# Optimization experiments

Hardware: AMD Instinct MI355X
Metric: run time of the kernel (lower is better)

The kernel has to match this reference:

```python
import jax, jax.numpy as jnp
import numpy as np

N_NODES = 100000
N_EDGES = 1600000
D_IN = 64
D_HID = 64
D_OUT = 64
DROP_P = 0.5


def _degree_norms(src, dst, n):
    ones = jnp.ones(src.shape[0], dtype=jnp.float32)
    deg_out = jax.ops.segment_sum(ones, src, num_segments=n)  # out-degree of src nodes
    deg_in = jax.ops.segment_sum(ones, dst, num_segments=n)   # in-degree of dst nodes
    norm_src = jnp.where(deg_out > 0, jax.lax.rsqrt(jnp.maximum(deg_out, 1.0)), 0.0)
    norm_dst = jnp.where(deg_in > 0, jax.lax.rsqrt(jnp.maximum(deg_in, 1.0)), 0.0)
    return norm_src, norm_dst


def _graph_conv(h, W, b, src, dst, norm_src, norm_dst, n, activation=None):
    # DGL GraphConv, norm='both': out = D_in^{-1/2} A (D_out^{-1/2} h) W + b
    h = h * norm_src[:, None]
    h = h @ W                      # small GEMM first (in >= out), math-equivalent
    msg = h[src]                   # gather  [E, d]
    agg = jax.ops.segment_sum(msg, dst, num_segments=n)  # scatter-add [N, d]
    out = agg * norm_dst[:, None] + b
    if activation is not None:
        out = activation(out)
    return out


def _dropout(h, key, p=DROP_P):
    keep = jax.random.bernoulli(key, 1.0 - p, h.shape)
    return jnp.where(keep, h / (1.0 - p), 0.0)


def setup_inputs() -> dict:
    key = jax.random.key(0)
    ks = jax.random.split(key, 6)
    x = jax.random.normal(ks[0], (N_NODES, D_IN), dtype=jnp.float32)
    W0 = jax.random.normal(ks[1], (D_IN, D_HID), dtype=jnp.float32) * 0.05
    W1 = jax.random.normal(ks[2], (D_HID, D_HID), dtype=jnp.float32) * 0.05
    W2 = jax.random.normal(ks[3], (D_HID, D_OUT), dtype=jnp.float32) * 0.05
    b0 = jnp.zeros((D_HID,), dtype=jnp.float32)
    b1 = jnp.zeros((D_HID,), dtype=jnp.float32)
    b2 = jnp.zeros((D_OUT,), dtype=jnp.float32)
    src = jax.random.randint(ks[4], (N_EDGES,), 0, N_NODES, dtype=jnp.int32)
    dst = jax.random.randint(ks[5], (N_EDGES,), 0, N_NODES, dtype=jnp.int32)
    return {"x": x, "W0": W0, "b0": b0, "W1": W1, "b1": b1, "W2": W2, "b2": b2,
            "src": src, "dst": dst}


def reference(x, W0, b0, W1, b1, W2, b2, src, dst):
    n = x.shape[0]
    norm_src, norm_dst = _degree_norms(src, dst, n)
    dk = jax.random.key(1)
    h = _graph_conv(x, W0, b0, src, dst, norm_src, norm_dst, n, jax.nn.relu)
    h = _dropout(h, jax.random.fold_in(dk, 0))
    h = _graph_conv(h, W1, b1, src, dst, norm_src, norm_dst, n, jax.nn.relu)
    h = _dropout(h, jax.random.fold_in(dk, 1))
    h = _graph_conv(h, W2, b2, src, dst, norm_src, norm_dst, n, None)
    return h
```

## Files before the change

kernel.cpp:

```cpp
#include <hip/hip_runtime.h>
#include <hip/hip_bf16.h>
#include <hip/hip_fp16.h>
#include <cstddef>


#define WG 256
#define WGB 512
#define WGD 1024
#define NWAVES (WGD / 64)
#define SLOT_S 48
#define NB_SHIFT 9
#define NB_W 512
#define EB 2048
#define PSTRIDE 257

__host__ __device__ static inline unsigned rotl32(unsigned x, int r) {
  return (x << r) | (x >> (32 - r));
}

__host__ __device__ static inline void threefry2x32(unsigned k0, unsigned k1,
                                                    unsigned x0, unsigned x1,
                                                    unsigned& o0, unsigned& o1) {
  unsigned ks2 = k0 ^ k1 ^ 0x1BD11BDAu;
  x0 += k0; x1 += k1;
#define TF_ROUND(r) { x0 += x1; x1 = rotl32(x1, r); x1 ^= x0; }
  TF_ROUND(13) TF_ROUND(15) TF_ROUND(26) TF_ROUND(6)
  x0 += k1;  x1 += ks2 + 1u;
  TF_ROUND(17) TF_ROUND(29) TF_ROUND(16) TF_ROUND(24)
  x0 += ks2; x1 += k0 + 2u;
  TF_ROUND(13) TF_ROUND(15) TF_ROUND(26) TF_ROUND(6)
  x0 += k0;  x1 += k1 + 3u;
  TF_ROUND(17) TF_ROUND(29) TF_ROUND(16) TF_ROUND(24)
  x0 += k1;  x1 += ks2 + 4u;
  TF_ROUND(13) TF_ROUND(15) TF_ROUND(26) TF_ROUND(6)
  x0 += ks2; x1 += k0 + 5u;
#undef TF_ROUND
  o0 = x0; o1 = x1;
}

__device__ static inline float2 h2f(unsigned u) {
  return __half22float2(__builtin_bit_cast(__half2, u));
}
__device__ static inline unsigned f2h(float a, float b) {
  return __builtin_bit_cast(unsigned, __floats2half2_rn(a, b));
}


__global__ __launch_bounds__(WGB) void bin_k(
    const int* __restrict__ src, const int* __restrict__ dst,
    unsigned* __restrict__ binbuf_d, unsigned short* __restrict__ binbuf_s,
    unsigned short* __restrict__ pref_d, unsigned short* __restrict__ pref_s,
    int e) {
  __shared__ int hist_d[256], hist_s[256];
  __shared__ int scan_d[256], scan_s[256];
  __shared__ int curs_d[256], curs_s[256];
  __shared__ unsigned sorted_d[EB];
  __shared__ unsigned short sorted_s[EB];
  int tid = threadIdx.x;
  int blk = blockIdx.x;
  int base = blk * EB;
  int cnt = e - base;
  if (cnt > EB) cnt = EB;

  if (tid < 256) { hist_d[tid] = 0; hist_s[tid] = 0; }
  __syncthreads();
  for (int i = tid; i < cnt; i += WGB) {
    int d = dst[base + i];
    int s = src[base + i];
    atomicAdd(&hist_d[d >> NB_SHIFT], 1);
    atomicAdd(&hist_s[s >> NB_SHIFT], 1);
  }
  __syncthreads();
  int hd = 0, hs = 0;
  if (tid < 256) {
    hd = hist_d[tid]; hs = hist_s[tid];
    scan_d[tid] = hd;
    scan_s[tid] = hs;
  }
  __syncthreads();
  for (int st = 1; st < 256; st <<= 1) {
    int ad = 0, as = 0;
    if (tid < 256 && tid >= st) { ad = scan_d[tid - st]; as = scan_s[tid - st]; }
    __syncthreads();
    if (tid < 256) { scan_d[tid] += ad; scan_s[tid] += as; }
    __syncthreads();
  }
  if (tid < 256) {
    int ed = scan_d[tid] - hd;
    int es = scan_s[tid] - hs;
    curs_d[tid] = ed;
    curs_s[tid] = es;
    pref_d[(size_t)blk * PSTRIDE + tid] = (unsigned short)ed;
    pref_s[(size_t)blk * PSTRIDE + tid] = (unsigned short)es;
    if (tid == 255) {
      pref_d[(size_t)blk * PSTRIDE + 256] = (unsigned short)scan_d[255];
      pref_s[(size_t)blk * PSTRIDE + 256] = (unsigned short)scan_s[255];
    }
  }
  __syncthreads();
  for (int i = tid; i < cnt; i += WGB) {
    int d = dst[base + i];
    int s = src[base + i];
    int pd = atomicAdd(&curs_d[d >> NB_SHIFT], 1);
    sorted_d[pd] = ((unsigned)(d & (NB_W - 1)) << 17) | (unsigned)s;
    int ps = atomicAdd(&curs_s[s >> NB_SHIFT], 1);
    sorted_s[ps] = (unsigned short)(s & (NB_W - 1));
  }
  __syncthreads();
  for (int i = tid; i < cnt; i += WGB) binbuf_d[base + i] = sorted_d[i];
  for (int i = tid; i < cnt; i += WGB) binbuf_s[base + i] = sorted_s[i];
}


__global__ __launch_bounds__(WGD) void debin_k(
    const unsigned* __restrict__ binbuf_d,
    const unsigned short* __restrict__ binbuf_s,
    const unsigned short* __restrict__ pref_d,
    const unsigned short* __restrict__ pref_s,
    int* __restrict__ slot, int* __restrict__ cnt_in,
    float* __restrict__ nsrc, int n, int nblk, int nwg) {
  __shared__ int lcnt[NB_W];
  int tid = threadIdx.x;
  int wave = tid >> 6;
  int lane = tid & 63;

  int j = blockIdx.x;
  int q = nwg >> 3, r = nwg & 7;
  int x = j & 7, p = j >> 3;
  int vb = (x < r ? x * (q + 1) : r * (q + 1) + (x - r) * q) + p;
  int role = vb & 1;
  int b = vb >> 1;

  for (int i = tid; i < NB_W; i += WGD) lcnt[i] = 0;
  __syncthreads();

  if (role == 0) {
    for (int seg = wave; seg < nblk; seg += NWAVES) {
      const unsigned short* pr = pref_d + (size_t)seg * PSTRIDE + b;
      int p0 = pr[0], p1 = pr[1];
      const unsigned* bb = binbuf_d + (size_t)seg * EB;
      for (int i = p0 + lane; i < p1; i += 64) {
        unsigned v = bb[i];
        int dl = v >> 17;
        int s = (int)(v & 0x1FFFFu);
        int c = atomicAdd(&lcnt[dl], 1);
        if (c < SLOT_S) slot[(size_t)((b << NB_SHIFT) + dl) * SLOT_S + c] = s;
      }
    }
    __syncthreads();
    for (int i = tid; i < NB_W; i += WGD) {
      int v = (b << NB_SHIFT) + i;
      if (v < n) cnt_in[v] = lcnt[i];
    }
  } else {
    for (int seg = wave; seg < nblk; seg += NWAVES) {
      const unsigned short* pr = pref_s + (size_t)seg * PSTRIDE + b;
      int p0 = pr[0], p1 = pr[1];
      const unsigned short* bb = binbuf_s + (size_t)seg * EB;
      for (int i = p0 + lane; i < p1; i += 64) atomicAdd(&lcnt[bb[i]], 1);
    }
    __syncthreads();
    int vbase = b << NB_SHIFT;
    for (int i = tid; i < NB_W; i += WGD) {
      int v = vbase + i;
      if (v < n) {
        int c = lcnt[i];
        nsrc[v] = (c > 0) ? rsqrtf((float)c) : 0.f;
      }
    }
  }
}


__global__ __launch_bounds__(WG) void ns_k(
    const float* __restrict__ nsrc, const float* __restrict__ x,
    unsigned short* __restrict__ G0, int n) {
  int idx = blockIdx.x * WG + threadIdx.x;
  int v = idx >> 4;
  if (v >= n) return;
  float ns = nsrc[v];
  float4 rr = ((const float4*)x)[(size_t)v * 16 + (idx & 15)];
  ((uint2*)G0)[(size_t)v * 16 + (idx & 15)] =
      make_uint2(f2h(rr.x * ns, rr.y * ns), f2h(rr.z * ns, rr.w * ns));
}


__global__ __launch_bounds__(WG) void agg_k(
    const unsigned short* __restrict__ G, const int* __restrict__ slot,
    const int* __restrict__ cnt_in, float* __restrict__ agg, int n) {
  int lane = threadIdx.x & 63;
  int g = lane >> 4;
  int l16 = lane & 15;
  int v = blockIdx.x * 16 + (threadIdx.x >> 6) * 4 + g;
  if (v >= n) return;

  int degt = cnt_in[v];
  int deg = (degt > SLOT_S) ? SLOT_S : degt;
  const int* sl = slot + (size_t)v * SLOT_S;
  const uint2* G2 = (const uint2*)G;

  float4 aA = make_float4(0.f, 0.f, 0.f, 0.f);
  float4 aB = make_float4(0.f, 0.f, 0.f, 0.f);
  float4 aC = make_float4(0.f, 0.f, 0.f, 0.f);
  float4 aD = make_float4(0.f, 0.f, 0.f, 0.f);
#define ACC(dst, m) { float2 lo = h2f((m).x), hi = h2f((m).y); \
    dst.x += lo.x; dst.y += lo.y; dst.z += hi.x; dst.w += hi.y; }
  int nq = deg >> 2;
  int i = 0;
  for (; i + 1 < nq; i += 2) {
    int4 q0 = *(const int4*)(sl + i * 4);
    int4 q1 = *(const int4*)(sl + i * 4 + 4);
    uint2 m0 = G2[(size_t)q0.x * 16 + l16];
    uint2 m1 = G2[(size_t)q0.y * 16 + l16];
    uint2 m2 = G2[(size_t)q0.z * 16 + l16];
    uint2 m3 = G2[(size_t)q0.w * 16 + l16];
    uint2 m4 = G2[(size_t)q1.x * 16 + l16];
    uint2 m5 = G2[(size_t)q1.y * 16 + l16];
    uint2 m6 = G2[(size_t)q1.z * 16 + l16];
    uint2 m7 = G2[(size_t)q1.w * 16 + l16];
    ACC(aA, m0) ACC(aB, m1) ACC(aC, m2) ACC(aD, m3)
    ACC(aA, m4) ACC(aB, m5) ACC(aC, m6) ACC(aD, m7)
  }
  if (i < nq) {
    int4 q0 = *(const int4*)(sl + i * 4);
    uint2 m0 = G2[(size_t)q0.x * 16 + l16];
    uint2 m1 = G2[(size_t)q0.y * 16 + l16];
    uint2 m2 = G2[(size_t)q0.z * 16 + l16];
    uint2 m3 = G2[(size_t)q0.w * 16 + l16];
    ACC(aA, m0) ACC(aB, m1) ACC(aC, m2) ACC(aD, m3)
  }
  int rem = deg & 3;
  if (rem) {
    int4 q = *(const int4*)(sl + (deg & ~3));
    int s0 = q.x;
    int s1 = (rem > 1) ? q.y : s0;
    int s2 = (rem > 2) ? q.z : s0;
    float w1 = (rem > 1) ? 1.f : 0.f;
    float w2 = (rem > 2) ? 1.f : 0.f;
    uint2 m0 = G2[(size_t)s0 * 16 + l16];
    uint2 m1 = G2[(size_t)s1 * 16 + l16];
    uint2 m2 = G2[(size_t)s2 * 16 + l16];
    ACC(aA, m0)
    { float2 lo = h2f(m1.x), hi = h2f(m1.y);
      aB.x = fmaf(w1, lo.x, aB.x); aB.y = fmaf(w1, lo.y, aB.y);
      aB.z = fmaf(w1, hi.x, aB.z); aB.w = fmaf(w1, hi.y, aB.w); }
    { float2 lo = h2f(m2.x), hi = h2f(m2.y);
      aC.x = fmaf(w2, lo.x, aC.x); aC.y = fmaf(w2, lo.y, aC.y);
      aC.z = fmaf(w2, hi.x, aC.z); aC.w = fmaf(w2, hi.y, aC.w); }
  }
#undef ACC
  float4 o;
  o.x = (aA.x + aB.x) + (aC.x + aD.x);
  o.y = (aA.y + aB.y) + (aC.y + aD.y);
  o.z = (aA.z + aB.z) + (aC.z + aD.z);
  o.w = (aA.w + aB.w) + (aC.w + aD.w);
  ((float4*)agg)[(size_t)v * 16 + l16] = o;
}


__global__ __launch_bounds__(WG) void gemm_k(
    const float* __restrict__ agg, const int* __restrict__ cnt_in,
    const float* __restrict__ nsrc, const float* __restrict__ W,
    const float* __restrict__ bias,
    unsigned short* __restrict__ GoutH, float* __restrict__ GoutF,
    int n, int mid, unsigned dk0, unsigned dk1) {
  __shared__ float4 Ws[1024];
  __shared__ __align__(16) float rows[4][272];
  const float4* W4 = (const float4*)W;
  for (int i = threadIdx.x; i < 1024; i += WG) Ws[i] = W4[i];

  int wave = threadIdx.x >> 6;
  int lane = threadIdx.x & 63;
  int g = lane >> 4;
  int l16 = lane & 15;
  int v = blockIdx.x * 16 + wave * 4 + g;
  bool valid = (v < n);
  int vc = valid ? v : (n - 1);

  int degt = valid ? cnt_in[vc] : 0;
  float4 a4 = ((const float4*)agg)[(size_t)vc * 16 + l16];

  float* rw = &rows[wave][g * 68];
  *(float4*)(rw + l16 * 4) = a4;
  __syncthreads();

  float4 acc = make_float4(0.f, 0.f, 0.f, 0.f);
#pragma unroll
  for (int k = 0; k < 64; ++k) {
    float a = rw[k];
    float4 w = Ws[k * 16 + l16];
    acc.x = fmaf(a, w.x, acc.x);
    acc.y = fmaf(a, w.y, acc.y);
    acc.z = fmaf(a, w.z, acc.z);
    acc.w = fmaf(a, w.w, acc.w);
  }

  float nd = (degt > 0) ? rsqrtf((float)degt) : 0.f;
  float4 b4 = ((const float4*)bias)[l16];
  float4 o;
  o.x = fmaf(acc.x, nd, b4.x);
  o.y = fmaf(acc.y, nd, b4.y);
  o.z = fmaf(acc.z, nd, b4.z);
  o.w = fmaf(acc.w, nd, b4.w);
  if (mid) {
    o.x = fmaxf(o.x, 0.f); o.y = fmaxf(o.y, 0.f);
    o.z = fmaxf(o.z, 0.f); o.w = fmaxf(o.w, 0.f);
    unsigned idx = (unsigned)(v * 64 + l16 * 4);
    unsigned r0a, r0b, r1a, r1b, r2a, r2b, r3a, r3b;
    threefry2x32(dk0, dk1, 0u, idx + 0u, r0a, r0b);
    threefry2x32(dk0, dk1, 0u, idx + 1u, r1a, r1b);
    threefry2x32(dk0, dk1, 0u, idx + 2u, r2a, r2b);
    threefry2x32(dk0, dk1, 0u, idx + 3u, r3a, r3b);
    float ns2 = 2.f * nsrc[vc];
    o.x = ((r0a ^ r0b) & 0x80000000u) ? 0.f : o.x * ns2;
    o.y = ((r1a ^ r1b) & 0x80000000u) ? 0.f : o.y * ns2;
    o.z = ((r2a ^ r2b) & 0x80000000u) ? 0.f : o.z * ns2;
    o.w = ((r3a ^ r3b) & 0x80000000u) ? 0.f : o.w * ns2;
    if (valid)
      ((uint2*)GoutH)[(size_t)v * 16 + l16] =
          make_uint2(f2h(o.x, o.y), f2h(o.z, o.w));
  } else {
    if (valid) ((float4*)GoutF)[(size_t)v * 16 + l16] = o;
  }
}


extern "C" void kernel_launch(void* const* d_in, const int* in_sizes, int n_in,
                              void* d_out, int out_size, void* d_ws, size_t ws_size,
                              hipStream_t stream) {
  const float* x  = (const float*)d_in[0];
  const float* W0 = (const float*)d_in[1];
  const float* b0 = (const float*)d_in[2];
  const float* W1 = (const float*)d_in[3];
  const float* b1 = (const float*)d_in[4];
  const float* W2 = (const float*)d_in[5];
  const float* b2 = (const float*)d_in[6];
  const int* src  = (const int*)d_in[7];
  const int* dst  = (const int*)d_in[8];
  float* out = (float*)d_out;

  const int n = in_sizes[0] / 64;
  const int e = in_sizes[7];
  const int nbuck = (n + NB_W - 1) / NB_W;
  const int nblk = (e + EB - 1) / EB;

  char* w = (char*)d_ws;
  size_t off = 0;
  auto alloc = [&](size_t bytes) -> void* {
    void* p = w + off;
    off += (bytes + 255) & ~(size_t)255;
    return p;
  };
  int*            cnt_in = (int*)alloc((size_t)n * 4);
  float*          nsrc   = (float*)alloc((size_t)n * 4);
  int*            slot   = (int*)alloc((size_t)nbuck * NB_W * SLOT_S * 4);
  unsigned short* G0     = (unsigned short*)alloc((size_t)n * 64 * 2);
  unsigned short* G1     = (unsigned short*)alloc((size_t)n * 64 * 2);

  size_t bd_sz = ((size_t)nblk * EB * 4 + 255) & ~(size_t)255;
  size_t bs_sz = ((size_t)nblk * EB * 2 + 255) & ~(size_t)255;
  size_t pf_sz = ((size_t)nblk * PSTRIDE * 2 + 255) & ~(size_t)255;
  size_t bin_total = bd_sz + bs_sz + 2 * pf_sz;
  size_t agg_sz = (size_t)n * 64 * 4;
  char* ubase = (char*)alloc(bin_total > agg_sz ? bin_total : agg_sz);
  unsigned*       binbuf_d = (unsigned*)ubase;
  unsigned short* binbuf_s = (unsigned short*)(ubase + bd_sz);
  unsigned short* pref_d   = (unsigned short*)(ubase + bd_sz + bs_sz);
  unsigned short* pref_s   = (unsigned short*)(ubase + bd_sz + bs_sz + pf_sz);
  float*          aggbuf   = (float*)ubase;

  unsigned k0a, k0b, k1a, k1b;
  threefry2x32(0u, 1u, 0u, 0u, k0a, k0b);
  threefry2x32(0u, 1u, 0u, 1u, k1a, k1b);

  const int gL = (n + 15) / 16;
  const int gN = (n * 16 + WG - 1) / WG;

  bin_k<<<nblk, WGB, 0, stream>>>(src, dst, binbuf_d, binbuf_s,
                                  pref_d, pref_s, e);
  debin_k<<<2 * nbuck, WGD, 0, stream>>>(binbuf_d, binbuf_s, pref_d, pref_s,
                                         slot, cnt_in, nsrc, n, nblk,
                                         2 * nbuck);
  ns_k<<<gN, WG, 0, stream>>>(nsrc, x, G0, n);

  agg_k<<<gL, WG, 0, stream>>>(G0, slot, cnt_in, aggbuf, n);
  gemm_k<<<gL, WG, 0, stream>>>(aggbuf, cnt_in, nsrc, W0, b0,
                                G1, nullptr, n, 1, k0a, k0b);
  agg_k<<<gL, WG, 0, stream>>>(G1, slot, cnt_in, aggbuf, n);
  gemm_k<<<gL, WG, 0, stream>>>(aggbuf, cnt_in, nsrc, W1, b1,
                                G0, nullptr, n, 1, k1a, k1b);
  agg_k<<<gL, WG, 0, stream>>>(G0, slot, cnt_in, aggbuf, n);
  gemm_k<<<gL, WG, 0, stream>>>(aggbuf, cnt_in, nsrc, W2, b2,
                                nullptr, out, n, 0, 0u, 0u);
}
```

Baseline: 312.5 us.

## Slice fp16 feature tables into 4 column slices pinned to XCD pairs

```diff
diff --git a/kernel.cpp b/kernel.cpp
--- a/kernel.cpp
+++ b/kernel.cpp
@@ -13,6 +13,8 @@
 #define NB_W 512
 #define EB 2048
 #define PSTRIDE 257
+#define NSLICE 4
+#define AGG_NPB 64
 
 __host__ __device__ static inline unsigned rotl32(unsigned x, int r) {
   return (x << r) | (x >> (32 - r));
@@ -178,31 +180,35 @@
   int idx = blockIdx.x * WG + threadIdx.x;
   int v = idx >> 4;
   if (v >= n) return;
+  int l16 = idx & 15;
   float ns = nsrc[v];
-  float4 rr = ((const float4*)x)[(size_t)v * 16 + (idx & 15)];
-  ((uint2*)G0)[(size_t)v * 16 + (idx & 15)] =
+  float4 rr = ((const float4*)x)[(size_t)v * 16 + l16];
+  ((uint2*)G0)[((size_t)(l16 >> 2) * n + v) * 4 + (l16 & 3)] =
       make_uint2(f2h(rr.x * ns, rr.y * ns), f2h(rr.z * ns, rr.w * ns));
 }
 
 
 __global__ __launch_bounds__(WG) void agg_k(
     const unsigned short* __restrict__ G, const int* __restrict__ slot,
-    const int* __restrict__ cnt_in, float* __restrict__ agg, int n) {
-  int lane = threadIdx.x & 63;
-  int g = lane >> 4;
-  int l16 = lane & 15;
-  int v = blockIdx.x * 16 + (threadIdx.x >> 6) * 4 + g;
+    const int* __restrict__ cnt_in, float* __restrict__ agg,
+    int n, int nchunk) {
+  int bid = blockIdx.x;
+  int xcd = bid & 7;
+  int s = xcd & 3;
+  int c = ((bid >> 3) << 1) | (xcd >> 2);
+  if (c >= nchunk) return;
+  int quad = threadIdx.x >> 2;
+  int lq = threadIdx.x & 3;
+  int v = c * AGG_NPB + quad;
   if (v >= n) return;
 
   int degt = cnt_in[v];
   int deg = (degt > SLOT_S) ? SLOT_S : degt;
   const int* sl = slot + (size_t)v * SLOT_S;
-  const uint2* G2 = (const uint2*)G;
+  const uint2* Gs = (const uint2*)G + (size_t)s * n * 4;
 
   float4 aA = make_float4(0.f, 0.f, 0.f, 0.f);
   float4 aB = make_float4(0.f, 0.f, 0.f, 0.f);
-  float4 aC = make_float4(0.f, 0.f, 0.f, 0.f);
-  float4 aD = make_float4(0.f, 0.f, 0.f, 0.f);
 #define ACC(dst, m) { float2 lo = h2f((m).x), hi = h2f((m).y); \
     dst.x += lo.x; dst.y += lo.y; dst.z += hi.x; dst.w += hi.y; }
   int nq = deg >> 2;
@@ -210,24 +216,24 @@
   for (; i + 1 < nq; i += 2) {
     int4 q0 = *(const int4*)(sl + i * 4);
     int4 q1 = *(const int4*)(sl + i * 4 + 4);
-    uint2 m0 = G2[(size_t)q0.x * 16 + l16];
-    uint2 m1 = G2[(size_t)q0.y * 16 + l16];
-    uint2 m2 = G2[(size_t)q0.z * 16 + l16];
-    uint2 m3 = G2[(size_t)q0.w * 16 + l16];
-    uint2 m4 = G2[(size_t)q1.x * 16 + l16];
-    uint2 m5 = G2[(size_t)q1.y * 16 + l16];
-    uint2 m6 = G2[(size_t)q1.z * 16 + l16];
-    uint2 m7 = G2[(size_t)q1.w * 16 + l16];
-    ACC(aA, m0) ACC(aB, m1) ACC(aC, m2) ACC(aD, m3)
-    ACC(aA, m4) ACC(aB, m5) ACC(aC, m6) ACC(aD, m7)
+    uint2 m0 = Gs[(size_t)q0.x * 4 + lq];
+    uint2 m1 = Gs[(size_t)q0.y * 4 + lq];
+    uint2 m2 = Gs[(size_t)q0.z * 4 + lq];
+    uint2 m3 = Gs[(size_t)q0.w * 4 + lq];
+    uint2 m4 = Gs[(size_t)q1.x * 4 + lq];
+    uint2 m5 = Gs[(size_t)q1.y * 4 + lq];
+    uint2 m6 = Gs[(size_t)q1.z * 4 + lq];
+    uint2 m7 = Gs[(size_t)q1.w * 4 + lq];
+    ACC(aA, m0) ACC(aB, m1) ACC(aA, m2) ACC(aB, m3)
+    ACC(aA, m4) ACC(aB, m5) ACC(aA, m6) ACC(aB, m7)
   }
   if (i < nq) {
     int4 q0 = *(const int4*)(sl + i * 4);
-    uint2 m0 = G2[(size_t)q0.x * 16 + l16];
-    uint2 m1 = G2[(size_t)q0.y * 16 + l16];
-    uint2 m2 = G2[(size_t)q0.z * 16 + l16];
-    uint2 m3 = G2[(size_t)q0.w * 16 + l16];
-    ACC(aA, m0) ACC(aB, m1) ACC(aC, m2) ACC(aD, m3)
+    uint2 m0 = Gs[(size_t)q0.x * 4 + lq];
+    uint2 m1 = Gs[(size_t)q0.y * 4 + lq];
+    uint2 m2 = Gs[(size_t)q0.z * 4 + lq];
+    uint2 m3 = Gs[(size_t)q0.w * 4 + lq];
+    ACC(aA, m0) ACC(aB, m1) ACC(aA, m2) ACC(aB, m3)
   }
   int rem = deg & 3;
   if (rem) {
@@ -237,24 +243,24 @@
     int s2 = (rem > 2) ? q.z : s0;
     float w1 = (rem > 1) ? 1.f : 0.f;
     float w2 = (rem > 2) ? 1.f : 0.f;
-    uint2 m0 = G2[(size_t)s0 * 16 + l16];
-    uint2 m1 = G2[(size_t)s1 * 16 + l16];
-    uint2 m2 = G2[(size_t)s2 * 16 + l16];
+    uint2 m0 = Gs[(size_t)s0 * 4 + lq];
+    uint2 m1 = Gs[(size_t)s1 * 4 + lq];
+    uint2 m2 = Gs[(size_t)s2 * 4 + lq];
     ACC(aA, m0)
     { float2 lo = h2f(m1.x), hi = h2f(m1.y);
       aB.x = fmaf(w1, lo.x, aB.x); aB.y = fmaf(w1, lo.y, aB.y);
       aB.z = fmaf(w1, hi.x, aB.z); aB.w = fmaf(w1, hi.y, aB.w); }
     { float2 lo = h2f(m2.x), hi = h2f(m2.y);
-      aC.x = fmaf(w2, lo.x, aC.x); aC.y = fmaf(w2, lo.y, aC.y);
-      aC.z = fmaf(w2, hi.x, aC.z); aC.w = fmaf(w2, hi.y, aC.w); }
+      aA.x = fmaf(w2, lo.x, aA.x); aA.y = fmaf(w2, lo.y, aA.y);
+      aA.z = fmaf(w2, hi.x, aA.z); aA.w = fmaf(w2, hi.y, aA.w); }
   }
 #undef ACC
   float4 o;
-  o.x = (aA.x + aB.x) + (aC.x + aD.x);
-  o.y = (aA.y + aB.y) + (aC.y + aD.y);
-  o.z = (aA.z + aB.z) + (aC.z + aD.z);
-  o.w = (aA.w + aB.w) + (aC.w + aD.w);
-  ((float4*)agg)[(size_t)v * 16 + l16] = o;
+  o.x = aA.x + aB.x;
+  o.y = aA.y + aB.y;
+  o.z = aA.z + aB.z;
+  o.w = aA.w + aB.w;
+  *(float4*)(agg + ((size_t)s * n + v) * 16 + lq * 4) = o;
 }
 
 
@@ -278,7 +284,8 @@
   int vc = valid ? v : (n - 1);
 
   int degt = valid ? cnt_in[vc] : 0;
-  float4 a4 = ((const float4*)agg)[(size_t)vc * 16 + l16];
+  float4 a4 = *(const float4*)(agg + ((size_t)(l16 >> 2) * n + vc) * 16 +
+                               (l16 & 3) * 4);
 
   float* rw = &rows[wave][g * 68];
   *(float4*)(rw + l16 * 4) = a4;
@@ -317,7 +324,7 @@
     o.z = ((r2a ^ r2b) & 0x80000000u) ? 0.f : o.z * ns2;
     o.w = ((r3a ^ r3b) & 0x80000000u) ? 0.f : o.w * ns2;
     if (valid)
-      ((uint2*)GoutH)[(size_t)v * 16 + l16] =
+      ((uint2*)GoutH)[((size_t)(l16 >> 2) * n + v) * 4 + (l16 & 3)] =
           make_uint2(f2h(o.x, o.y), f2h(o.z, o.w));
   } else {
     if (valid) ((float4*)GoutF)[(size_t)v * 16 + l16] = o;
@@ -375,6 +382,8 @@
 
   const int gL = (n + 15) / 16;
   const int gN = (n * 16 + WG - 1) / WG;
+  const int nchunk = (n + AGG_NPB - 1) / AGG_NPB;
+  const int gA = 8 * ((nchunk + 1) / 2);
 
   bin_k<<<nblk, WGB, 0, stream>>>(src, dst, binbuf_d, binbuf_s,
                                   pref_d, pref_s, e);
@@ -383,13 +392,13 @@
                                          2 * nbuck);
   ns_k<<<gN, WG, 0, stream>>>(nsrc, x, G0, n);
 
-  agg_k<<<gL, WG, 0, stream>>>(G0, slot, cnt_in, aggbuf, n);
+  agg_k<<<gA, WG, 0, stream>>>(G0, slot, cnt_in, aggbuf, n, nchunk);
   gemm_k<<<gL, WG, 0, stream>>>(aggbuf, cnt_in, nsrc, W0, b0,
                                 G1, nullptr, n, 1, k0a, k0b);
-  agg_k<<<gL, WG, 0, stream>>>(G1, slot, cnt_in, aggbuf, n);
+  agg_k<<<gA, WG, 0, stream>>>(G1, slot, cnt_in, aggbuf, n, nchunk);
   gemm_k<<<gL, WG, 0, stream>>>(aggbuf, cnt_in, nsrc, W1, b1,
                                 G0, nullptr, n, 1, k1a, k1b);
-  agg_k<<<gL, WG, 0, stream>>>(G0, slot, cnt_in, aggbuf, n);
+  agg_k<<<gA, WG, 0, stream>>>(G0, slot, cnt_in, aggbuf, n, nchunk);
   gemm_k<<<gL, WG, 0, stream>>>(aggbuf, cnt_in, nsrc, W2, b2,
                                 nullptr, out, n, 0, 0u, 0u);
 }
```

New measurement: 364.2 us. +16.6%, slower.
